# Kernel tuning notes

Hardware: AMD Instinct MI355X
Metric: run time of the kernel (lower is better)

Reference implementation:

```python
import jax, jax.numpy as jnp
import numpy as np

HIDDEN = 1024

def setup_inputs() -> dict:
    key = jax.random.key(0)
    ks = jax.random.split(key, 4)
    scale = 1.0 / np.sqrt(HIDDEN)
    return {
        "X": jax.random.normal(ks[0], (4, 4096, HIDDEN), dtype=jnp.float32),
        "Wq": jax.random.normal(ks[1], (HIDDEN, HIDDEN), dtype=jnp.float32) * scale,
        "bq": jnp.zeros((HIDDEN,), dtype=jnp.float32),
        "Wk": jax.random.normal(ks[2], (HIDDEN, HIDDEN), dtype=jnp.float32) * scale,
        "bk": jnp.zeros((HIDDEN,), dtype=jnp.float32),
        "Wv": jax.random.normal(ks[3], (HIDDEN, HIDDEN), dtype=jnp.float32) * scale,
        "bv": jnp.zeros((HIDDEN,), dtype=jnp.float32),
    }

def reference(X, Wq, bq, Wk, bk, Wv, bv):
    # nn.Linear: x @ W.T + b
    Q = jnp.einsum("bsh,dh->bsd", X, Wq) + bq   # [B,S,H]
    K = jnp.einsum("bsh,dh->bsd", X, Wk) + bk
    V = jnp.einsum("bsh,dh->bsd", X, Wv) + bv
    scores = jnp.einsum("bsd,btd->bst", Q, K) / jnp.sqrt(jnp.asarray(X.shape[-1], X.dtype))  # [B,S,S]
    attn = jax.nn.softmax(scores, axis=-1)
    return jnp.einsum("bst,btd->bsd", attn, V)  # [B,S,H]
```

## Files before the change

### kernel.cpp

```cpp
#include <hip/hip_runtime.h>
#include <math.h>

#define HIDDEN 1024
#define SEQ    4096
#define BATCH  4

typedef _Float16 f16x8 __attribute__((ext_vector_type(8)));
typedef float    floatx4 __attribute__((ext_vector_type(4)));

__device__ inline void gld16(const void* g, void* l) {
    __builtin_amdgcn_global_load_lds(
        (const __attribute__((address_space(1))) unsigned int*)g,
        (__attribute__((address_space(3))) unsigned int*)l, 16, 0, 0);
}

template<int MODE, int NT>
__global__ __launch_bounds__(512)
void gemm256_kernel(const _Float16* __restrict__ A,
                    const _Float16* __restrict__ Bq,
                    const _Float16* __restrict__ Bk,
                    const _Float16* __restrict__ Bv,
                    const float* __restrict__ bq,
                    const float* __restrict__ bk,
                    const float* __restrict__ bv,
                    float alpha,
                    _Float16* __restrict__ Eo,
                    _Float16* __restrict__ Qo,
                    _Float16* __restrict__ Ko,
                    _Float16* __restrict__ Vo,
                    float* __restrict__ Cf,
                    float* __restrict__ Lsum) {
    constexpr int LDAB = (MODE == 4) ? SEQ : HIDDEN;
    __shared__ __align__(16) char smem[65536];
    char* sA = smem;
    char* sB = smem + 32768;

    const int tid  = threadIdx.x;
    const int lane = tid & 63;
    const int w    = tid >> 6;
    const int wm   = w & 1;
    const int wn   = w >> 1;
    const int quad = lane >> 4;
    const int l16  = lane & 15;
    const int swz  = (l16 >> 1) & 3;

    int row0, col0, z = 0;
    if constexpr (MODE == 5) {
        const int n = blockIdx.x, xcd = n & 7, slot = n >> 3;
        const int cc = slot % 12, rg = xcd + 8 * (slot / 12);
        row0 = rg * 256; col0 = cc * 256;
    } else if constexpr (MODE == 3) {
        z = blockIdx.y;
        const int bx = blockIdx.x, wgid = (bx & 7) * 32 + (bx >> 3);
        row0 = (wgid >> 4) * 256; col0 = (wgid & 15) * 256;
    } else {
        z = blockIdx.y;
        const int n = blockIdx.x, xcd = n & 7, slot = n >> 3;
        const int cc = slot & 3, rg = xcd + 8 * (slot >> 2);
        row0 = rg * 256; col0 = cc * 256;
    }

    const _Float16* Abase;
    const _Float16* Bbase;
    int colbase = col0, which = 0;
    if constexpr (MODE == 5) {
        which = col0 >> 10; colbase = col0 & 1023;
        const _Float16* Bsrc = (which == 0) ? Bq : (which == 1) ? Bk : Bv;
        Abase = A + (size_t)row0 * HIDDEN;
        Bbase = Bsrc + (size_t)colbase * HIDDEN;
    } else if constexpr (MODE == 3) {
        Abase = A  + (size_t)z * SEQ * HIDDEN + (size_t)row0 * HIDDEN;
        Bbase = Bq + (size_t)z * SEQ * HIDDEN + (size_t)col0 * HIDDEN;
        Eo   += (size_t)z * SEQ * SEQ;
        Lsum += (size_t)z * SEQ;
    } else {
        Abase = A  + (size_t)z * SEQ * SEQ    + (size_t)row0 * SEQ;
        Bbase = Bq + (size_t)z * HIDDEN * SEQ + (size_t)col0 * SEQ;
        Cf   += (size_t)z * SEQ * HIDDEN;
        Lsum += (size_t)z * SEQ;
    }

    const int n0 = tid, n1 = tid + 512;
    const int r0s = n0 >> 2, p0s = n0 & 3;
    const int r1s = n1 >> 2, p1s = n1 & 3;
    const int off0 = r0s * LDAB + (p0s ^ ((r0s >> 1) & 3)) * 8;
    const int off1 = r1s * LDAB + (p1s ^ ((r1s >> 1) & 3)) * 8;

    auto stage = [&](const _Float16* base, char* lh, int kt) {
        const int kb = kt * 32;
        gld16(base + off0 + kb, lh + n0 * 16);
        gld16(base + off1 + kb, lh + n1 * 16);
    };

    floatx4 acc[8][4];
    #pragma unroll
    for (int i = 0; i < 8; ++i)
        #pragma unroll
        for (int j = 0; j < 4; ++j) acc[i][j] = (floatx4){0.f, 0.f, 0.f, 0.f};

    f16x8 afA[4], afB[4], bfX[4];

#define RD_AF(DST, RH, B_)                                                    \
  { const f16x8* pAh = (const f16x8*)(sA + (B_) * 16384);                     \
    _Pragma("unroll")                                                         \
    for (int i = 0; i < 4; ++i)                                               \
      DST[i] = pAh[(wm * 128 + (RH) * 64 + i * 16 + l16) * 4 + (quad ^ swz)]; }

#define RD_BF(DST, B_)                                                        \
  { const f16x8* pBh = (const f16x8*)(sB + (B_) * 16384);                     \
    _Pragma("unroll")                                                         \
    for (int j = 0; j < 4; ++j)                                               \
      DST[j] = pBh[(wn * 64 + j * 16 + l16) * 4 + (quad ^ swz)]; }

#define MM(RH, AF, BF)                                                        \
  __builtin_amdgcn_sched_barrier(0);                                          \
  __builtin_amdgcn_s_setprio(1);                                              \
  _Pragma("unroll")                                                           \
  for (int j = 0; j < 4; ++j)                                                 \
    _Pragma("unroll")                                                         \
    for (int i = 0; i < 4; ++i)                                               \
      acc[(RH) * 4 + i][j] = __builtin_amdgcn_mfma_f32_16x16x32_f16(          \
          AF[i], BF[j], acc[(RH) * 4 + i][j], 0, 0, 0);                       \
  __builtin_amdgcn_s_setprio(0);

#define QTILE(T_, STG)                                                        \
  { const int b_ = (T_) & 1, nb_ = b_ ^ 1;                                    \
    asm volatile("s_waitcnt vmcnt(0)" ::: "memory");                          \
    __builtin_amdgcn_s_barrier();                                             \
    RD_AF(afA, 0, b_);                                                        \
    RD_BF(bfX, b_);                                                           \
    RD_AF(afB, 1, b_);                                                        \
    if (STG) stage(Abase, sA + nb_ * 16384, (T_) + 1);                        \
    MM(0, afA, bfX)                                                           \
    if (STG) stage(Bbase, sB + nb_ * 16384, (T_) + 1);                        \
    MM(1, afB, bfX)                                                           \
  }

    stage(Abase, sA, 0);
    stage(Bbase, sB, 0);

    #pragma unroll 2
    for (int t = 0; t < NT - 1; ++t) QTILE(t, 1)
    QTILE(NT - 1, 0)

#undef QTILE
#undef MM
#undef RD_BF
#undef RD_AF

    #pragma unroll
    for (int i = 0; i < 8; ++i) {
        const int r0 = row0 + wm * 128 + i * 16 + quad * 4;
        if constexpr (MODE == 3) {
            float rp[4] = {0.f, 0.f, 0.f, 0.f};
            #pragma unroll
            for (int j = 0; j < 4; ++j) {
                const int cl = col0 + wn * 64 + j * 16 + l16;
                #pragma unroll
                for (int reg = 0; reg < 4; ++reg) {
                    const float v = exp2f(alpha * acc[i][j][reg] - 5.770780163555856f);
                    const _Float16 vh = (_Float16)v;
                    Eo[(size_t)(r0 + reg) * SEQ + cl] = vh;
                    rp[reg] += (float)vh;
                }
            }
            #pragma unroll
            for (int off = 1; off < 16; off <<= 1)
                #pragma unroll
                for (int reg = 0; reg < 4; ++reg)
                    rp[reg] += __shfl_xor(rp[reg], off, 64);
            if (l16 == 0)
                #pragma unroll
                for (int reg = 0; reg < 4; ++reg)
                    atomicAdd(&Lsum[r0 + reg], rp[reg]);
        } else if constexpr (MODE == 5) {
            #pragma unroll
            for (int j = 0; j < 4; ++j) {
                const int cl = colbase + wn * 64 + j * 16 + l16;
                const float bcol = (which == 0 ? bq : which == 1 ? bk : bv)[cl];
                if (which < 2) {
                    _Float16* O = (which == 0) ? Qo : Ko;
                    #pragma unroll
                    for (int reg = 0; reg < 4; ++reg)
                        O[(size_t)(r0 + reg) * HIDDEN + cl] =
                            (_Float16)(acc[i][j][reg] + bcol);
                } else {
                    const int bb = r0 >> 12;
                    const int s  = r0 & 4095;
                    _Float16 tq[4];
                    #pragma unroll
                    for (int reg = 0; reg < 4; ++reg)
                        tq[reg] = (_Float16)(acc[i][j][reg] + bcol);
                    *(uint2*)&Vo[((size_t)bb * HIDDEN + cl) * SEQ + s] = *(const uint2*)tq;
                }
            }
        } else {
            float linv[4];
            #pragma unroll
            for (int reg = 0; reg < 4; ++reg) linv[reg] = 1.0f / Lsum[r0 + reg];
            #pragma unroll
            for (int j = 0; j < 4; ++j) {
                const int cl = col0 + wn * 64 + j * 16 + l16;
                #pragma unroll
                for (int reg = 0; reg < 4; ++reg)
                    Cf[(size_t)(r0 + reg) * HIDDEN + cl] = acc[i][j][reg] * linv[reg];
            }
        }
    }
}

__global__ __launch_bounds__(256)
void cast_x_kernel(const float* __restrict__ in, _Float16* __restrict__ out) {
    const int i = blockIdx.x * 256 + threadIdx.x;
    const float4 x = ((const float4*)in)[i];
    _Float16 h[4] = {(_Float16)x.x, (_Float16)x.y, (_Float16)x.z, (_Float16)x.w};
    ((uint2*)out)[i] = *(const uint2*)h;
}

__global__ __launch_bounds__(256)
void cast_w_kernel(const float* __restrict__ w0, const float* __restrict__ w1,
                   const float* __restrict__ w2,
                   _Float16* __restrict__ o0, _Float16* __restrict__ o1,
                   _Float16* __restrict__ o2) {
    const float* in = (blockIdx.z == 0) ? w0 : (blockIdx.z == 1) ? w1 : w2;
    _Float16* out   = (blockIdx.z == 0) ? o0 : (blockIdx.z == 1) ? o1 : o2;
    const int i = blockIdx.x * 256 + threadIdx.x;
    const float4 x = ((const float4*)in)[i];
    _Float16 h[4] = {(_Float16)x.x, (_Float16)x.y, (_Float16)x.z, (_Float16)x.w};
    ((uint2*)out)[i] = *(const uint2*)h;
}

extern "C" void kernel_launch(void* const* d_in, const int* in_sizes, int n_in,
                              void* d_out, int out_size, void* d_ws, size_t ws_size,
                              hipStream_t stream) {
    const float* X  = (const float*)d_in[0];
    const float* Wq = (const float*)d_in[1];
    const float* bq = (const float*)d_in[2];
    const float* Wk = (const float*)d_in[3];
    const float* bk = (const float*)d_in[4];
    const float* Wv = (const float*)d_in[5];
    const float* bv = (const float*)d_in[6];
    float* out = (float*)d_out;

    char* ws = (char*)d_ws;
    const size_t EB = (size_t)BATCH * SEQ * SEQ * 2;
    const size_t XB = (size_t)BATCH * SEQ * HIDDEN * 2;
    const size_t WB = (size_t)HIDDEN * HIDDEN * 2;

    _Float16* E   = (_Float16*)ws;
    _Float16* Xh  = (_Float16*)ws;
    _Float16* Wqh = (_Float16*)(ws + XB);
    _Float16* Wkh = (_Float16*)(ws + XB + WB);
    _Float16* Wvh = (_Float16*)(ws + XB + 2 * WB);
    _Float16* Qh  = (_Float16*)(ws + EB);
    _Float16* Kh  = (_Float16*)(ws + EB + XB);
    _Float16* Vt  = (_Float16*)(ws + EB + 2 * XB);
    float*    Lsum= (float*)   (ws + EB + 3 * XB);

    cast_x_kernel<<<dim3(16384), dim3(256), 0, stream>>>(X, Xh);
    cast_w_kernel<<<dim3(1024, 1, 3), dim3(256), 0, stream>>>(
        Wq, Wk, Wv, Wqh, Wkh, Wvh);

    hipMemsetAsync(Lsum, 0, (size_t)BATCH * SEQ * sizeof(float), stream);

    gemm256_kernel<5, 32><<<dim3(768), dim3(512), 0, stream>>>(
        Xh, Wqh, Wkh, Wvh, bq, bk, bv, 0.f,
        nullptr, Qh, Kh, Vt, nullptr, nullptr);

    const float alpha2 = (1.0f / 32.0f) * 1.4426950408889634f;
    gemm256_kernel<3, 32><<<dim3(256, 4), dim3(512), 0, stream>>>(
        Qh, Kh, nullptr, nullptr, nullptr, nullptr, nullptr, alpha2,
        E, nullptr, nullptr, nullptr, nullptr, Lsum);

    gemm256_kernel<4, 128><<<dim3(64, 4), dim3(512), 0, stream>>>(
        E, Vt, nullptr, nullptr, nullptr, nullptr, nullptr, 0.f,
        nullptr, nullptr, nullptr, nullptr, out, Lsum);
}
```

Measured before the change: 518.9 us.

## Triple-buffer LDS tiles and prefetch fragments one stage ahead in GEMM

Replaces the double-buffered LDS pipeline with three A and B buffers, 96KB of LDS in total. Global loads are issued two k-tiles ahead and waited on with a partial vmcnt instead of a full drain. The LDS-to-register fragment reads for the next tile now happen after the current MFMAs, so they overlap with compute. It also drops the sched_barrier and setprio hints and adds a second-block occupancy hint to the launch bounds. The larger LDS footprint may limit how many blocks fit on a CU.

```diff
diff --git a/kernel.cpp b/kernel.cpp
--- a/kernel.cpp
+++ b/kernel.cpp
@@ -15,7 +15,7 @@
 }
 
 template<int MODE, int NT>
-__global__ __launch_bounds__(512)
+__global__ __launch_bounds__(512, 2)
 void gemm256_kernel(const _Float16* __restrict__ A,
                     const _Float16* __restrict__ Bq,
                     const _Float16* __restrict__ Bk,
@@ -31,9 +31,13 @@
                     float* __restrict__ Cf,
                     float* __restrict__ Lsum) {
     constexpr int LDAB = (MODE == 4) ? SEQ : HIDDEN;
-    __shared__ __align__(16) char smem[65536];
-    char* sA = smem;
-    char* sB = smem + 32768;
+    __shared__ __align__(16) char smem[98304];
+    char* const sA0 = smem;
+    char* const sA1 = smem + 16384;
+    char* const sA2 = smem + 32768;
+    char* const sB0 = smem + 49152;
+    char* const sB1 = smem + 65536;
+    char* const sB2 = smem + 81920;
 
     const int tid  = threadIdx.x;
     const int lane = tid & 63;
@@ -100,50 +104,58 @@
 
     f16x8 afA[4], afB[4], bfX[4];
 
-#define RD_AF(DST, RH, B_)                                                    \
-  { const f16x8* pAh = (const f16x8*)(sA + (B_) * 16384);                     \
+#define RD_AF(DST, RH, PBUF)                                                  \
+  { const f16x8* pAh = (const f16x8*)(PBUF);                                  \
     _Pragma("unroll")                                                         \
     for (int i = 0; i < 4; ++i)                                               \
       DST[i] = pAh[(wm * 128 + (RH) * 64 + i * 16 + l16) * 4 + (quad ^ swz)]; }
 
-#define RD_BF(DST, B_)                                                        \
-  { const f16x8* pBh = (const f16x8*)(sB + (B_) * 16384);                     \
+#define RD_BF(DST, PBUF)                                                      \
+  { const f16x8* pBh = (const f16x8*)(PBUF);                                  \
     _Pragma("unroll")                                                         \
     for (int j = 0; j < 4; ++j)                                               \
       DST[j] = pBh[(wn * 64 + j * 16 + l16) * 4 + (quad ^ swz)]; }
 
 #define MM(RH, AF, BF)                                                        \
-  __builtin_amdgcn_sched_barrier(0);                                          \
-  __builtin_amdgcn_s_setprio(1);                                              \
   _Pragma("unroll")                                                           \
   for (int j = 0; j < 4; ++j)                                                 \
     _Pragma("unroll")                                                         \
     for (int i = 0; i < 4; ++i)                                               \
       acc[(RH) * 4 + i][j] = __builtin_amdgcn_mfma_f32_16x16x32_f16(          \
-          AF[i], BF[j], acc[(RH) * 4 + i][j], 0, 0, 0);                       \
-  __builtin_amdgcn_s_setprio(0);
-
-#define QTILE(T_, STG)                                                        \
-  { const int b_ = (T_) & 1, nb_ = b_ ^ 1;                                    \
-    asm volatile("s_waitcnt vmcnt(0)" ::: "memory");                          \
+          AF[i], BF[j], acc[(RH) * 4 + i][j], 0, 0, 0);
+
+#define QT(AN, BN, AX, BX, KT2, STG, W)                                       \
+  { if (STG) { stage(Abase, AX, KT2); stage(Bbase, BX, KT2); }                \
+    asm volatile("s_waitcnt vmcnt(" W ")" ::: "memory");                      \
     __builtin_amdgcn_s_barrier();                                             \
-    RD_AF(afA, 0, b_);                                                        \
-    RD_BF(bfX, b_);                                                           \
-    RD_AF(afB, 1, b_);                                                        \
-    if (STG) stage(Abase, sA + nb_ * 16384, (T_) + 1);                        \
+    asm volatile("" ::: "memory");                                            \
     MM(0, afA, bfX)                                                           \
-    if (STG) stage(Bbase, sB + nb_ * 16384, (T_) + 1);                        \
     MM(1, afB, bfX)                                                           \
-  }
-
-    stage(Abase, sA, 0);
-    stage(Bbase, sB, 0);
-
-    #pragma unroll 2
-    for (int t = 0; t < NT - 1; ++t) QTILE(t, 1)
-    QTILE(NT - 1, 0)
-
-#undef QTILE
+    RD_AF(afA, 0, AN)                                                         \
+    RD_BF(bfX, BN)                                                            \
+    RD_AF(afB, 1, AN) }
+
+    stage(Abase, sA0, 0);
+    stage(Bbase, sB0, 0);
+    stage(Abase, sA1, 1);
+    stage(Bbase, sB1, 1);
+    asm volatile("s_waitcnt vmcnt(4)" ::: "memory");
+    __builtin_amdgcn_s_barrier();
+    asm volatile("" ::: "memory");
+    RD_AF(afA, 0, sA0)
+    RD_BF(bfX, sB0)
+    RD_AF(afB, 1, sA0)
+
+    for (int t = 0; t < NT - 2; t += 3) {
+        QT(sA1, sB1, sA2, sB2, t + 2, 1, "4")
+        QT(sA2, sB2, sA0, sB0, t + 3, 1, "4")
+        QT(sA0, sB0, sA1, sB1, t + 4, 1, "4")
+    }
+    QT(sA1, sB1, sA2, sB2, 0, 0, "0")
+    MM(0, afA, bfX)
+    MM(1, afB, bfX)
+
+#undef QT
 #undef MM
 #undef RD_BF
 #undef RD_AF
```

Measured after the change: 518.3 us. About the same (-0.1%).
